# Optimization experiments

Hardware: AMD Instinct MI355X
Metric: run time of the kernel (lower is better)

## Reference

```python
import jax, jax.numpy as jnp
import numpy as np

N_MEM = 8
B = 64
D_K = 256
D_V = 256


def setup_inputs() -> dict:
    key0 = jax.random.key(0)
    ks = jax.random.split(key0, 7)
    INIT_SCALE = 0.01
    return {
        "states": jax.random.normal(ks[0], (N_MEM, B, D_K, D_V), dtype=jnp.float32) * INIT_SCALE,
        "key": jax.random.normal(ks[1], (B, D_K), dtype=jnp.float32),
        "value": jax.random.normal(ks[2], (B, D_V), dtype=jnp.float32),
        "alpha": jax.random.uniform(ks[3], (B, 1), dtype=jnp.float32),
        "rho": jax.random.uniform(ks[4], (B, N_MEM), dtype=jnp.float32),
        "lam": jax.random.uniform(ks[5], (B, N_MEM), dtype=jnp.float32),
        "query": jax.random.normal(ks[6], (B, D_K), dtype=jnp.float32),
    }


def reference(states, key, value, alpha, rho, lam, query):
    # One MOM step: update every memory slot, then read every slot.
    # update: M_i = lam[:, i] * M_i + (rho[:, i] * alpha) * (k outer v)
    outer = jnp.einsum("bk,bv->bkv", key, value)              # [B, Dk, Dv]
    lam_s = lam.T[:, :, None, None]                            # [N, B, 1, 1]
    write_s = (rho * alpha).T[:, :, None, None]                # [N, B, 1, 1]
    new_states = lam_s * states + write_s * outer[None]        # [N, B, Dk, Dv]
    # read: r_i = q^T M_i  -> [N, B, Dv]
    readouts = jnp.einsum("bk,nbkv->nbv", query, new_states)
    return new_states, readouts
```

## Files before the change

kernel.cpp:

```cpp
#include <hip/hip_runtime.h>

#define N_MEM 8
#define BSZ   64
#define DK    256
#define DV    256

typedef float f32x4 __attribute__((ext_vector_type(4)));

__global__ __launch_bounds__(1024) void mom_kernel(
    const float* __restrict__ states,
    const float* __restrict__ key,
    const float* __restrict__ value,
    const float* __restrict__ alpha,
    const float* __restrict__ rho,
    const float* __restrict__ lam,
    const float* __restrict__ query,
    float* __restrict__ out_states,
    float* __restrict__ out_read)
{
    const int bid = blockIdx.x;
    const int n   = bid >> 6;
    const int b   = bid & 63;
    const int t   = threadIdx.x;

    __shared__ float s_key[DK];
    __shared__ float s_q[DK];
    __shared__ f32x4 s_val4[DV / 4];
    __shared__ f32x4 s_red[1024];

    if (t < DK) {
        s_key[t] = key[b * DK + t];
        s_q[t]   = query[b * DK + t];
    } else if (t < DK + DV / 4) {
        const int v4 = t - DK;
        s_val4[v4] = reinterpret_cast<const f32x4*>(value + (size_t)b * DV)[v4];
    }
    const float lam_s = lam[b * N_MEM + n];
    const float w_s   = rho[b * N_MEM + n] * alpha[b];
    __syncthreads();

    const int   v4  = t & 63;
    const f32x4 val = s_val4[v4];
    const int   k0  = t >> 6;

    float kw[16], qv[16];
#pragma unroll
    for (int it = 0; it < 16; ++it) {
        kw[it] = w_s * s_key[k0 + it * 16];
        qv[it] = s_q[k0 + it * 16];
    }

    const size_t base = (size_t)bid * (DK * DV);
    const f32x4* __restrict__ sp = reinterpret_cast<const f32x4*>(states + base);
    f32x4*       __restrict__ op = reinterpret_cast<f32x4*>(out_states + base);

    f32x4 racc = (f32x4)(0.f);

#pragma unroll
    for (int it = 0; it < 16; ++it) {
        const int idx = t + it * 1024;
        const f32x4 s = sp[idx];
        const f32x4 ns = lam_s * s + kw[it] * val;
        __builtin_nontemporal_store(ns, &op[idx]);
        racc += qv[it] * ns;
    }

    s_red[t] = racc;
    __syncthreads();
    if (t < 64) {
        f32x4 acc = s_red[t];
#pragma unroll
        for (int g = 1; g < 16; ++g)
            acc += s_red[t + g * 64];
        reinterpret_cast<f32x4*>(out_read + (size_t)bid * DV)[t] = acc;
    }
}

extern "C" void kernel_launch(void* const* d_in, const int* in_sizes, int n_in,
                              void* d_out, int out_size, void* d_ws, size_t ws_size,
                              hipStream_t stream) {
    const float* states = (const float*)d_in[0];
    const float* key    = (const float*)d_in[1];
    const float* value  = (const float*)d_in[2];
    const float* alpha  = (const float*)d_in[3];
    const float* rho    = (const float*)d_in[4];
    const float* lam    = (const float*)d_in[5];
    const float* query  = (const float*)d_in[6];

    float* out_states = (float*)d_out;
    float* out_read   = out_states + (size_t)N_MEM * BSZ * DK * DV;

    dim3 grid(N_MEM * BSZ);
    dim3 block(1024);
    mom_kernel<<<grid, block, 0, stream>>>(states, key, value, alpha, rho, lam,
                                           query, out_states, out_read);
}
```

Baseline: 48.16 us.

## Split each memory slot across four 256-thread blocks with a separate partial-sum reduce

Each (slot, batch) state matrix is split into four 64-row chunks, each handled by a 256-thread block. Every block writes a partial readout to workspace, and a second small kernel sums the four partials. This gives 2048 blocks instead of 512 for better load balance and occupancy across CUs on a memory-bound streaming kernel. The cost is a second kernel launch and an extra workspace round trip. The code falls back to the monolithic kernel when the workspace is too small.

```diff
diff --git a/kernel.cpp b/kernel.cpp
--- a/kernel.cpp
+++ b/kernel.cpp
@@ -7,7 +7,7 @@
 
 typedef float f32x4 __attribute__((ext_vector_type(4)));
 
-__global__ __launch_bounds__(1024) void mom_kernel(
+__global__ __launch_bounds__(256) void mom_kernel_fine(
     const float* __restrict__ states,
     const float* __restrict__ key,
     const float* __restrict__ value,
@@ -16,6 +16,88 @@
     const float* __restrict__ lam,
     const float* __restrict__ query,
     float* __restrict__ out_states,
+    float* __restrict__ ws_partial)
+{
+    const int bid4  = blockIdx.x;
+    const int group = bid4 >> 2;
+    const int chunk = bid4 & 3;
+    const int n     = group >> 6;
+    const int b     = group & 63;
+    const int t     = threadIdx.x;
+
+    __shared__ float s_key[64];
+    __shared__ float s_q[64];
+    __shared__ f32x4 s_val4[DV / 4];
+    __shared__ f32x4 s_red[256];
+
+    if (t < 64) {
+        const int kg = chunk * 64 + t;
+        s_key[t] = key[b * DK + kg];
+        s_q[t]   = query[b * DK + kg];
+    } else if (t < 128) {
+        const int v4 = t - 64;
+        s_val4[v4] = reinterpret_cast<const f32x4*>(value + (size_t)b * DV)[v4];
+    }
+    const float lam_s = lam[b * N_MEM + n];
+    const float w_s   = rho[b * N_MEM + n] * alpha[b];
+    __syncthreads();
+
+    const int   v4  = t & 63;
+    const f32x4 val = s_val4[v4];
+    const int   k0  = t >> 6;
+
+    float kw[16], qv[16];
+#pragma unroll
+    for (int it = 0; it < 16; ++it) {
+        kw[it] = w_s * s_key[k0 + it * 4];
+        qv[it] = s_q[k0 + it * 4];
+    }
+
+    const size_t base = (size_t)group * (DK * DV) + (size_t)chunk * (64 * DV);
+    const f32x4* __restrict__ sp = reinterpret_cast<const f32x4*>(states + base);
+    f32x4*       __restrict__ op = reinterpret_cast<f32x4*>(out_states + base);
+
+    f32x4 racc = (f32x4)(0.f);
+
+#pragma unroll
+    for (int it = 0; it < 16; ++it) {
+        const int idx = t + it * 256;
+        const f32x4 s  = sp[idx];
+        const f32x4 ns = lam_s * s + kw[it] * val;
+        __builtin_nontemporal_store(ns, &op[idx]);
+        racc += qv[it] * ns;
+    }
+
+    s_red[t] = racc;
+    __syncthreads();
+    if (t < 64) {
+        f32x4 acc = s_red[t];
+#pragma unroll
+        for (int g = 1; g < 4; ++g)
+            acc += s_red[t + g * 64];
+        reinterpret_cast<f32x4*>(ws_partial + (size_t)bid4 * DV)[t] = acc;
+    }
+}
+
+__global__ __launch_bounds__(64) void mom_reduce(
+    const float* __restrict__ ws_partial,
+    float* __restrict__ out_read)
+{
+    const int g = blockIdx.x;
+    const int t = threadIdx.x;
+    const f32x4* wp = reinterpret_cast<const f32x4*>(ws_partial);
+    f32x4 acc = (f32x4)(0.f);
+#pragma unroll
+    for (int c = 0; c < 4; ++c)
+        acc += wp[(size_t)(g * 4 + c) * (DV / 4) + t];
+    reinterpret_cast<f32x4*>(out_read)[(size_t)g * (DV / 4) + t] = acc;
+}
+
+__global__ __launch_bounds__(1024) void mom_kernel_mono(
+    const float* __restrict__ states, const float* __restrict__ key,
+    const float* __restrict__ value, const float* __restrict__ alpha,
+    const float* __restrict__ rho, const float* __restrict__ lam,
+    const float* __restrict__ query, float* __restrict__ out_states,
     float* __restrict__ out_read)
 {
     const int bid = blockIdx.x;
@@ -32,8 +114,7 @@
         s_key[t] = key[b * DK + t];
         s_q[t]   = query[b * DK + t];
     } else if (t < DK + DV / 4) {
-        const int v4 = t - DK;
-        s_val4[v4] = reinterpret_cast<const f32x4*>(value + (size_t)b * DV)[v4];
+        s_val4[t - DK] = reinterpret_cast<const f32x4*>(value + (size_t)b * DV)[t - DK];
     }
     const float lam_s = lam[b * N_MEM + n];
     const float w_s   = rho[b * N_MEM + n] * alpha[b];
@@ -55,11 +136,10 @@
     f32x4*       __restrict__ op = reinterpret_cast<f32x4*>(out_states + base);
 
     f32x4 racc = (f32x4)(0.f);
-
 #pragma unroll
     for (int it = 0; it < 16; ++it) {
         const int idx = t + it * 1024;
-        const f32x4 s = sp[idx];
+        const f32x4 s  = sp[idx];
         const f32x4 ns = lam_s * s + kw[it] * val;
         __builtin_nontemporal_store(ns, &op[idx]);
         racc += qv[it] * ns;
@@ -90,8 +170,14 @@
     float* out_states = (float*)d_out;
     float* out_read   = out_states + (size_t)N_MEM * BSZ * DK * DV;
 
-    dim3 grid(N_MEM * BSZ);
-    dim3 block(1024);
-    mom_kernel<<<grid, block, 0, stream>>>(states, key, value, alpha, rho, lam,
-                                           query, out_states, out_read);
+    const size_t need_ws = (size_t)2048 * DV * sizeof(float);
+    if (ws_size >= need_ws) {
+        float* ws_partial = (float*)d_ws;
+        mom_kernel_fine<<<dim3(2048), dim3(256), 0, stream>>>(
+            states, key, value, alpha, rho, lam, query, out_states, ws_partial);
+        mom_reduce<<<dim3(512), dim3(64), 0, stream>>>(ws_partial, out_read);
+    } else {
+        mom_kernel_mono<<<dim3(512), dim3(1024), 0, stream>>>(
+            states, key, value, alpha, rho, lam, query, out_states, out_read);
+    }
 }
```

Result: faster. 46.79 us (-2.8%).

## Split each state slab across four 256-thread blocks with atomic readout reduction

Applied to the files above, without the earlier changes.

Each (n,b) slab is now handled by four 256-thread blocks instead of one 1024-thread block, each covering 64 key rows. Partial readouts are combined with float atomicAdd into an output zeroed beforehand by an added memset. Loads are batched in groups of eight to raise memory-level parallelism. The aim is finer-grained scheduling and better occupancy on a bandwidth-bound kernel, at the cost of an extra memset launch, atomics, and a summation order that can vary between runs.

```diff
diff --git a/kernel.cpp b/kernel.cpp
--- a/kernel.cpp
+++ b/kernel.cpp
@@ -7,7 +7,7 @@
 
 typedef float f32x4 __attribute__((ext_vector_type(4)));
 
-__global__ __launch_bounds__(1024) void mom_kernel(
+__global__ __launch_bounds__(256) void mom_kernel_fine(
     const float* __restrict__ states,
     const float* __restrict__ key,
     const float* __restrict__ value,
@@ -18,21 +18,24 @@
     float* __restrict__ out_states,
     float* __restrict__ out_read)
 {
-    const int bid = blockIdx.x;
-    const int n   = bid >> 6;
-    const int b   = bid & 63;
-    const int t   = threadIdx.x;
+    const int bid4  = blockIdx.x;
+    const int group = bid4 >> 2;
+    const int chunk = bid4 & 3;
+    const int n     = group >> 6;
+    const int b     = group & 63;
+    const int t     = threadIdx.x;
 
-    __shared__ float s_key[DK];
-    __shared__ float s_q[DK];
+    __shared__ float s_key[64];
+    __shared__ float s_q[64];
     __shared__ f32x4 s_val4[DV / 4];
-    __shared__ f32x4 s_red[1024];
+    __shared__ f32x4 s_red[256];
 
-    if (t < DK) {
-        s_key[t] = key[b * DK + t];
-        s_q[t]   = query[b * DK + t];
-    } else if (t < DK + DV / 4) {
-        const int v4 = t - DK;
+    if (t < 64) {
+        const int kg = chunk * 64 + t;
+        s_key[t] = key[b * DK + kg];
+        s_q[t]   = query[b * DK + kg];
+    } else if (t < 128) {
+        const int v4 = t - 64;
         s_val4[v4] = reinterpret_cast<const f32x4*>(value + (size_t)b * DV)[v4];
     }
     const float lam_s = lam[b * N_MEM + n];
@@ -43,26 +46,34 @@
     const f32x4 val = s_val4[v4];
     const int   k0  = t >> 6;
 
-    float kw[16], qv[16];
-#pragma unroll
-    for (int it = 0; it < 16; ++it) {
-        kw[it] = w_s * s_key[k0 + it * 16];
-        qv[it] = s_q[k0 + it * 16];
-    }
-
-    const size_t base = (size_t)bid * (DK * DV);
+    const size_t base = (size_t)group * (DK * DV) + (size_t)chunk * (64 * DV);
     const f32x4* __restrict__ sp = reinterpret_cast<const f32x4*>(states + base);
     f32x4*       __restrict__ op = reinterpret_cast<f32x4*>(out_states + base);
 
     f32x4 racc = (f32x4)(0.f);
 
 #pragma unroll
-    for (int it = 0; it < 16; ++it) {
-        const int idx = t + it * 1024;
-        const f32x4 s = sp[idx];
-        const f32x4 ns = lam_s * s + kw[it] * val;
-        __builtin_nontemporal_store(ns, &op[idx]);
-        racc += qv[it] * ns;
+    for (int half = 0; half < 2; ++half) {
+        f32x4 s[8];
+#pragma unroll
+        for (int j = 0; j < 8; ++j)
+            s[j] = sp[t + (half * 8 + j) * 256];
+
+        float kw8[8], qv8[8];
+#pragma unroll
+        for (int j = 0; j < 8; ++j) {
+            const int it = half * 8 + j;
+            kw8[j] = w_s * s_key[k0 + it * 4];
+            qv8[j] = s_q[k0 + it * 4];
+        }
+
+#pragma unroll
+        for (int j = 0; j < 8; ++j) {
+            const int it = half * 8 + j;
+            const f32x4 ns = lam_s * s[j] + kw8[j] * val;
+            __builtin_nontemporal_store(ns, &op[t + it * 256]);
+            racc += qv8[j] * ns;
+        }
     }
 
     s_red[t] = racc;
@@ -70,9 +81,13 @@
     if (t < 64) {
         f32x4 acc = s_red[t];
 #pragma unroll
-        for (int g = 1; g < 16; ++g)
+        for (int g = 1; g < 4; ++g)
             acc += s_red[t + g * 64];
-        reinterpret_cast<f32x4*>(out_read + (size_t)bid * DV)[t] = acc;
+        float* dst = out_read + (size_t)group * DV + t * 4;
+        atomicAdd(dst + 0, acc.x);
+        atomicAdd(dst + 1, acc.y);
+        atomicAdd(dst + 2, acc.z);
+        atomicAdd(dst + 3, acc.w);
     }
 }
 
@@ -90,8 +105,8 @@
     float* out_states = (float*)d_out;
     float* out_read   = out_states + (size_t)N_MEM * BSZ * DK * DV;
 
-    dim3 grid(N_MEM * BSZ);
-    dim3 block(1024);
-    mom_kernel<<<grid, block, 0, stream>>>(states, key, value, alpha, rho, lam,
-                                           query, out_states, out_read);
+    hipMemsetAsync(out_read, 0, (size_t)N_MEM * BSZ * DV * sizeof(float), stream);
+
+    mom_kernel_fine<<<dim3(2048), dim3(256), 0, stream>>>(
+        states, key, value, alpha, rho, lam, query, out_states, out_read);
 }
```

Result: slower. 51.18 us (+6.3%).
